# Optimization experiments

Hardware: AMD Instinct MI355X
Metric: run time of the kernel (lower is better)

The kernel has to match this reference:

```python
import jax, jax.numpy as jnp
import numpy as np

B, S, D = 2, 2048, 2048
NH, NG = 16, 4          # q heads, groups
KVH = NH // NG          # kv heads = 4
HD = D // NH            # head dim = 128
ROPE_THETA = 10000.0


def _rope(t, cos, sin):
    """Rotate pairs along last dim. t: [B,S,D]; cos/sin: [S, D//2]."""
    tr = t.reshape(t.shape[:-1] + (-1, 2))  # [B,S,D/2,2] complex pairs (llama layout)
    xr, xi = tr[..., 0], tr[..., 1]
    c = cos[None, :, :]
    s = sin[None, :, :]
    yr = xr * c - xi * s
    yi = xr * s + xi * c
    return jnp.stack([yr, yi], axis=-1).reshape(t.shape)


def setup_inputs() -> dict:
    key = jax.random.key(0)
    k0, k1, k2, k3, k4 = jax.random.split(key, 5)
    scale = 1.0 / np.sqrt(D)
    x = jax.random.normal(k0, (B, S, D), jnp.float32)
    Wq = jax.random.normal(k1, (D, D), jnp.float32) * scale          # torch Linear: (out,in)
    Wk = jax.random.normal(k2, (D // NG, D), jnp.float32) * scale
    Wv = jax.random.normal(k3, (D // NG, D), jnp.float32) * scale
    Wo = jax.random.normal(k4, (D, D), jnp.float32) * scale
    mask = jnp.triu(jnp.ones((S, S), bool), k=1)[None, None]          # causal: True = masked
    return {"x": x, "Wq": Wq, "Wk": Wk, "Wv": Wv, "Wo": Wo, "mask": mask}


def reference(x, Wq, Wk, Wv, Wo, mask):
    b, s, d = x.shape
    q = x @ Wq.T                                  # [B,S,D]
    k = x @ Wk.T                                  # [B,S,D/NG]
    v = x @ Wv.T
    # repeat_kv: [B,S,KVH,HD] -> repeat each kv head NG times -> [B,S,NH,HD]
    k = jnp.repeat(k.reshape(b, s, KVH, HD), NG, axis=2).reshape(b, s, d)
    v = jnp.repeat(v.reshape(b, s, KVH, HD), NG, axis=2).reshape(b, s, d)
    # RoPE with freqs precomputed over the FULL hidden dim (as in source)
    freqs = 1.0 / (ROPE_THETA ** (jnp.arange(0, d, 2, dtype=jnp.float32) / d))  # [D/2]
    ang = jnp.arange(s, dtype=jnp.float32)[:, None] * freqs[None, :]            # [S,D/2]
    cos, sin = jnp.cos(ang), jnp.sin(ang)
    q = _rope(q, cos, sin)
    k = _rope(k, cos, sin)
    # split heads: [B,NH,S,HD]
    qh = q.reshape(b, s, NH, HD).transpose(0, 2, 1, 3)
    kh = k.reshape(b, s, NH, HD).transpose(0, 2, 1, 3)
    vh = v.reshape(b, s, NH, HD).transpose(0, 2, 1, 3)
    # NOTE: source scales by sqrt(hidden_dim), not sqrt(head_dim)
    scores = jnp.einsum('bhqd,bhkd->bhqk', qh, kh) / jnp.sqrt(jnp.float32(d))
    scores = jnp.where(mask, -jnp.inf, scores)
    probs = jax.nn.softmax(scores, axis=-1)
    out = jnp.einsum('bhqk,bhkd->bhqd', probs, vh)
    out = out.transpose(0, 2, 1, 3).reshape(b, s, d)
    return out @ Wo.T  # dropout is identity in eval
```

## Files before the change

### kernel.cpp

```cpp
#include <hip/hip_runtime.h>
#include <hip/hip_bf16.h>
#include <stdint.h>

typedef unsigned short u16;
typedef u16 u16x4 __attribute__((ext_vector_type(4)));
typedef unsigned u32x4 __attribute__((ext_vector_type(4)));
typedef __bf16 bf16x8 __attribute__((ext_vector_type(8)));
typedef float f32x4 __attribute__((ext_vector_type(4)));
typedef float f32x16 __attribute__((ext_vector_type(16)));

#define DEVI __device__ __forceinline__

DEVI u16 f2b(float f) {
  __hip_bfloat16 h = __float2bfloat16(f);
  return __builtin_bit_cast(u16, h);
}

DEVI unsigned pk2(float lo, float hi) {
  return (unsigned)f2b(lo) | ((unsigned)f2b(hi) << 16);
}

DEVI f32x4 mfma16(bf16x8 a, bf16x8 b, f32x4 c) {
  return __builtin_amdgcn_mfma_f32_16x16x32_bf16(a, b, c, 0, 0, 0);
}

DEVI f32x16 mfma32(bf16x8 a, bf16x8 b, f32x16 c) {
  return __builtin_amdgcn_mfma_f32_32x32x16_bf16(a, b, c, 0, 0, 0);
}

DEVI void gld_lds16(const u16* g, u16* l) {
  __builtin_amdgcn_global_load_lds(
      (const __attribute__((address_space(1))) unsigned int*)g,
      (__attribute__((address_space(3))) unsigned int*)l, 16, 0, 0);
}

__global__ void cvt_all(const float4* __restrict__ x, const float4* __restrict__ wq,
                        const float4* __restrict__ wk, const float4* __restrict__ wv,
                        const float4* __restrict__ wo,
                        u16x4* __restrict__ xb, u16x4* __restrict__ wqb,
                        u16x4* __restrict__ wkb, u16x4* __restrict__ wvb,
                        u16x4* __restrict__ wob) {
  long i = (long)blockIdx.x * 256 + threadIdx.x;
  const float4* src; u16x4* dst; long o;
  if (i < 2097152)      { src = x;  dst = xb;  o = i; }
  else if (i < 3145728) { src = wq; dst = wqb; o = i - 2097152; }
  else if (i < 3407872) { src = wk; dst = wkb; o = i - 3145728; }
  else if (i < 3670016) { src = wv; dst = wvb; o = i - 3407872; }
  else                  { src = wo; dst = wob; o = i - 3670016; }
  float4 v = src[o];
  u16x4 r = { f2b(v.x), f2b(v.y), f2b(v.z), f2b(v.w) };
  dst[o] = r;
}

__global__ void rope_table(float* __restrict__ cosT, float* __restrict__ sinT) {
  int i = blockIdx.x * 256 + threadIdx.x;
  int s = i >> 10, p = i & 1023;
  float freq = exp2f((float)p * -0.012976281620653759f);
  float ang = (float)s * freq;
  float sv, cv;
  __sincosf(ang, &sv, &cv);
  cosT[i] = cv;
  sinT[i] = sv;
}

__global__ __launch_bounds__(256)
void gemm_qkv(const u16* __restrict__ A, const u16* __restrict__ wq,
              const u16* __restrict__ wk, const u16* __restrict__ wv,
              float* __restrict__ Qtmp, float* __restrict__ Ktmp,
              u16* __restrict__ Vtp) {
  __shared__ __align__(16) u16 lds[2][2][4096];
  const int tid = threadIdx.x;
  const int lane = tid & 63;
  const int w = tid >> 6;
  const int wr = w >> 1, wc = w & 1;
  const int bx = blockIdx.x;
  const int m0 = blockIdx.y << 7, n0 = bx << 7;
  const int K = 2048;

  const u16* Bw;
  int mode;
  if (bx < 16)      { Bw = wq + (size_t)n0 * K;          mode = 0; }
  else if (bx < 20) { Bw = wk + (size_t)(n0 - 2048) * K; mode = 1; }
  else              { Bw = wv + (size_t)(n0 - 2560) * K; mode = 2; }

  const int srow = tid >> 2;
  const int schunk = (tid & 3) << 3;
  const u16* ga0 = A + (size_t)(m0 + srow) * K + schunk;
  const u16* gb0 = Bw + (size_t)srow * K + schunk;
  const size_t rstep = (size_t)64 * K;

  f32x4 acc[4][4] = {};
  const int nk = K >> 5;
  int cur = 0;

  {
    u16* la = &lds[0][0][tid << 3];
    u16* lb = &lds[0][1][tid << 3];
    gld_lds16(ga0, la);
    gld_lds16(ga0 + rstep, la + 2048);
    gld_lds16(gb0, lb);
    gld_lds16(gb0 + rstep, lb + 2048);
  }
  __syncthreads();

  const int l15 = lane & 15;
  const int kcol = (lane >> 4) << 3;
  const int arow = ((wr << 6) + l15) << 5;
  const int brow = ((wc << 6) + l15) << 5;

  for (int kt = 0; kt < nk; ++kt) {
    if (kt + 1 < nk) {
      const u16* ga = ga0 + ((size_t)(kt + 1) << 5);
      const u16* gb = gb0 + ((size_t)(kt + 1) << 5);
      u16* la = &lds[cur ^ 1][0][tid << 3];
      u16* lb = &lds[cur ^ 1][1][tid << 3];
      gld_lds16(ga, la);
      gld_lds16(ga + rstep, la + 2048);
      gld_lds16(gb, lb);
      gld_lds16(gb + rstep, lb + 2048);
    }
    const u16* la = &lds[cur][0][0];
    const u16* lb = &lds[cur][1][0];
    bf16x8 af[4], bfr[4];
#pragma unroll
    for (int mi = 0; mi < 4; ++mi)
      af[mi] = *(const bf16x8*)&la[arow + (mi << 9) + kcol];
#pragma unroll
    for (int ni = 0; ni < 4; ++ni)
      bfr[ni] = *(const bf16x8*)&lb[brow + (ni << 9) + kcol];
#pragma unroll
    for (int mi = 0; mi < 4; ++mi)
#pragma unroll
      for (int ni = 0; ni < 4; ++ni)
        acc[mi][ni] = mfma16(af[mi], bfr[ni], acc[mi][ni]);
    __syncthreads();
    cur ^= 1;
  }

  const int crow = (lane >> 4) << 2;
  const int ccol = lane & 15;
  if (mode == 0) {
#pragma unroll
    for (int mi = 0; mi < 4; ++mi) {
      int row = m0 + (wr << 6) + (mi << 4) + crow;
#pragma unroll
      for (int ni = 0; ni < 4; ++ni) {
        int col = n0 + (wc << 6) + (ni << 4) + ccol;
#pragma unroll
        for (int rr = 0; rr < 4; ++rr)
          Qtmp[(size_t)(row + rr) * 2048 + col] = acc[mi][ni][rr];
      }
    }
  } else if (mode == 1) {
#pragma unroll
    for (int mi = 0; mi < 4; ++mi) {
      int row = m0 + (wr << 6) + (mi << 4) + crow;
#pragma unroll
      for (int ni = 0; ni < 4; ++ni) {
        int col = (n0 - 2048) + (wc << 6) + (ni << 4) + ccol;
#pragma unroll
        for (int rr = 0; rr < 4; ++rr)
          Ktmp[(size_t)(row + rr) * 512 + col] = acc[mi][ni][rr];
      }
    }
  } else {
#pragma unroll
    for (int mi = 0; mi < 4; ++mi) {
      int sg = m0 + (wr << 6) + (mi << 4) + crow;
      int b = sg >> 11, s = sg & 2047;
#pragma unroll
      for (int ni = 0; ni < 4; ++ni) {
        int n = (n0 - 2560) + (wc << 6) + (ni << 4) + ccol;
        u16x4 pk = { f2b(acc[mi][ni][0]), f2b(acc[mi][ni][1]),
                     f2b(acc[mi][ni][2]), f2b(acc[mi][ni][3]) };
        *(u16x4*)&Vtp[((size_t)((b << 2) + (n >> 7)) * 128 + (n & 127)) * 2048 + s] = pk;
      }
    }
  }
}

__global__ __launch_bounds__(256)
void gemm_bt(const u16* __restrict__ A, const u16* __restrict__ Bw,
             float* __restrict__ C, int M, int N, int K) {
  __shared__ __align__(16) u16 lds[2][2][4096];
  const int tid = threadIdx.x;
  const int lane = tid & 63;
  const int w = tid >> 6;
  const int wr = w >> 1, wc = w & 1;
  const int m0 = blockIdx.y << 7, n0 = blockIdx.x << 7;

  const int srow = tid >> 2;
  const int schunk = (tid & 3) << 3;
  const u16* ga0 = A + (size_t)(m0 + srow) * K + schunk;
  const u16* gb0 = Bw + (size_t)(n0 + srow) * K + schunk;
  const size_t rstep = (size_t)64 * K;

  f32x4 acc[4][4] = {};
  const int nk = K >> 5;
  int cur = 0;

  {
    u16* la = &lds[0][0][tid << 3];
    u16* lb = &lds[0][1][tid << 3];
    gld_lds16(ga0, la);
    gld_lds16(ga0 + rstep, la + 2048);
    gld_lds16(gb0, lb);
    gld_lds16(gb0 + rstep, lb + 2048);
  }
  __syncthreads();

  const int l15 = lane & 15;
  const int kcol = (lane >> 4) << 3;
  const int arow = ((wr << 6) + l15) << 5;
  const int brow = ((wc << 6) + l15) << 5;

  for (int kt = 0; kt < nk; ++kt) {
    if (kt + 1 < nk) {
      const u16* ga = ga0 + ((size_t)(kt + 1) << 5);
      const u16* gb = gb0 + ((size_t)(kt + 1) << 5);
      u16* la = &lds[cur ^ 1][0][tid << 3];
      u16* lb = &lds[cur ^ 1][1][tid << 3];
      gld_lds16(ga, la);
      gld_lds16(ga + rstep, la + 2048);
      gld_lds16(gb, lb);
      gld_lds16(gb + rstep, lb + 2048);
    }
    const u16* la = &lds[cur][0][0];
    const u16* lb = &lds[cur][1][0];
    bf16x8 af[4], bfr[4];
#pragma unroll
    for (int mi = 0; mi < 4; ++mi)
      af[mi] = *(const bf16x8*)&la[arow + (mi << 9) + kcol];
#pragma unroll
    for (int ni = 0; ni < 4; ++ni)
      bfr[ni] = *(const bf16x8*)&lb[brow + (ni << 9) + kcol];
#pragma unroll
    for (int mi = 0; mi < 4; ++mi)
#pragma unroll
      for (int ni = 0; ni < 4; ++ni)
        acc[mi][ni] = mfma16(af[mi], bfr[ni], acc[mi][ni]);
    __syncthreads();
    cur ^= 1;
  }

  const int crow = (lane >> 4) << 2;
  const int ccol = lane & 15;
#pragma unroll
  for (int mi = 0; mi < 4; ++mi) {
    int row = m0 + (wr << 6) + (mi << 4) + crow;
#pragma unroll
    for (int ni = 0; ni < 4; ++ni) {
      int col = n0 + (wc << 6) + (ni << 4) + ccol;
#pragma unroll
      for (int rr = 0; rr < 4; ++rr)
        C[(size_t)(row + rr) * N + col] = acc[mi][ni][rr];
    }
  }
}

__global__ void rope_q(const float2* __restrict__ Qtmp, const float* __restrict__ cosT,
                       const float* __restrict__ sinT, u16* __restrict__ Qh) {
  int i = blockIdx.x * 256 + threadIdx.x;
  int pr = i & 1023;
  int row = i >> 10;
  int s = row & 2047, b = row >> 11;
  float2 v = Qtmp[(size_t)row * 1024 + pr];
  float c = cosT[(s << 10) + pr], sn = sinT[(s << 10) + pr];
  const float SC = 0.022097086912079608f * 1.4426950408889634f;
  float yr = (v.x * c - v.y * sn) * SC;
  float yi = (v.x * sn + v.y * c) * SC;
  int h = pr >> 6, hp = pr & 63;
  size_t off = ((size_t)(b * 16 + h) * 2048 + s) * 128 + hp * 2;
  unsigned pk = (unsigned)f2b(yr) | ((unsigned)f2b(yi) << 16);
  *(unsigned*)&Qh[off] = pk;
}

__global__ void rope_k(const float2* __restrict__ Ktmp, const float* __restrict__ cosT,
                       const float* __restrict__ sinT, u16* __restrict__ Kh) {
  int i = blockIdx.x * 256 + threadIdx.x;
  int hp = i & 63;
  int h = (i >> 6) & 15;
  int row = i >> 10;
  int s = row & 2047, b = row >> 11;
  float2 v = Ktmp[(size_t)row * 256 + ((h >> 2) << 6) + hp];
  int p = (h << 6) + hp;
  float c = cosT[(s << 10) + p], sn = sinT[(s << 10) + p];
  float yr = v.x * c - v.y * sn;
  float yi = v.x * sn + v.y * c;
  size_t off = ((size_t)(b * 16 + h) * 2048 + s) * 128 + hp * 2;
  unsigned pk = (unsigned)f2b(yr) | ((unsigned)f2b(yi) << 16);
  *(unsigned*)&Kh[off] = pk;
}

__global__ __launch_bounds__(256, 2)
void attn_kernel(const u16* __restrict__ Qh, const u16* __restrict__ Kh,
                 const u16* __restrict__ Vt, u16* __restrict__ attnO) {
  __shared__ __align__(16) u16 lds[3][8192];
  const int tid = threadIdx.x, lane = tid & 63, w = tid >> 6;
  const int bid = blockIdx.x;
  const int x = bid & 7, j = bid >> 3;
  const int half = j >> 5, jj = j & 31;
  const int bh = (x << 2) + (jj >> 4) + (half << 1);
  const int r = jj & 15;
  const int qt = half ? r : 15 - r;
  const int h = bh & 15, b = bh >> 4;

  const int qi = lane & 31, hi = lane >> 5;
  const int q0 = (qt << 7) + (w << 5);
  const int qabs = q0 + qi;

  const u16* Qp = Qh + (size_t)(b * 16 + h) * 262144;
  const u16* Kp = Kh + (size_t)(b * 16 + h) * 262144;
  const u16* Vp = Vt + (size_t)((b << 2) + (h >> 2)) * 262144;

  bf16x8 qf[8];
#pragma unroll
  for (int kc = 0; kc < 8; ++kc)
    qf[kc] = *(const bf16x8*)&Qp[(size_t)qabs * 128 + kc * 16 + hi * 8];

  const int kRow = tid >> 4;
  const int kCl = ((tid & 15) ^ (kRow & 7)) << 3;
  const int vRow = tid >> 2;
  const int vCl = ((tid & 3) ^ ((tid >> 3) & 3)) << 3;
  const int ldsoff = tid << 3;

  f32x16 ot[4] = {};
  float mrow = -1e30f, lsum = 0.f;
  const int nt = (qt << 2) + 4;
  const int nt_w = (qt << 2) + w + 1;
  const int swq = qi & 7, swv = (qi >> 1) & 3;

#pragma unroll
  for (int pt = 0; pt < 2; ++pt) {
    u16* bb = (u16*)lds[pt];
    gld_lds16(Kp + (size_t)((pt << 5) + kRow) * 128 + kCl, bb + ldsoff);
    gld_lds16(Kp + (size_t)((pt << 5) + kRow + 16) * 128 + kCl, bb + ldsoff + 2048);
    gld_lds16(Vp + (size_t)vRow * 2048 + (pt << 5) + vCl, bb + 4096 + ldsoff);
    gld_lds16(Vp + (size_t)(vRow + 64) * 2048 + (pt << 5) + vCl, bb + 4096 + ldsoff + 2048);
  }

  int bufc = 0;
  for (int t = 0; t < nt; ++t) {
    asm volatile("s_waitcnt vmcnt(4)" ::: "memory");
    __builtin_amdgcn_sched_barrier(0);
    __builtin_amdgcn_s_barrier();
    {
      const int ts = (t + 2 < nt) ? t + 2 : nt - 1;
      const int bufn = bufc ? bufc - 1 : 2;
      u16* bb = (u16*)lds[bufn];
      gld_lds16(Kp + (size_t)((ts << 5) + kRow) * 128 + kCl, bb + ldsoff);
      gld_lds16(Kp + (size_t)((ts << 5) + kRow + 16) * 128 + kCl, bb + ldsoff + 2048);
      gld_lds16(Vp + (size_t)vRow * 2048 + (ts << 5) + vCl, bb + 4096 + ldsoff);
      gld_lds16(Vp + (size_t)(vRow + 64) * 2048 + (ts << 5) + vCl, bb + 4096 + ldsoff + 2048);
    }
    if (t < nt_w) {
      const u16* kb_ = &lds[bufc][0];
      const u16* vb_ = &lds[bufc][4096];
      f32x16 st = {};
      __builtin_amdgcn_s_setprio(1);
#pragma unroll
      for (int kc = 0; kc < 8; ++kc) {
        bf16x8 kf = *(const bf16x8*)&kb_[(qi << 7) + ((((kc << 1) + hi) ^ swq) << 3)];
        st = mfma32(kf, qf[kc], st);
      }
      __builtin_amdgcn_s_setprio(0);

      if (t == nt_w - 1) {
        const int kb0 = t << 5;
#pragma unroll
        for (int reg = 0; reg < 16; ++reg) {
          int kk = kb0 + (reg & 3) + ((reg >> 2) << 3) + (hi << 2);
          if (kk > qabs) st[reg] = -1e30f;
        }
      }

      float tmax = st[0];
#pragma unroll
      for (int reg = 1; reg < 16; ++reg) tmax = fmaxf(tmax, st[reg]);
      tmax = fmaxf(tmax, __shfl_xor(tmax, 32));

      if (__any(tmax - mrow > 11.5f)) {
        float nm = fmaxf(mrow, tmax);
        float al = __builtin_amdgcn_exp2f(mrow - nm);
        mrow = nm;
        lsum *= al;
#pragma unroll
        for (int db = 0; db < 4; ++db)
#pragma unroll
          for (int reg = 0; reg < 16; ++reg) ot[db][reg] *= al;
      }

      float psum = 0.f;
#pragma unroll
      for (int reg = 0; reg < 16; ++reg) {
        st[reg] = __builtin_amdgcn_exp2f(st[reg] - mrow);
        psum += st[reg];
      }
      psum += __shfl_xor(psum, 32);
      lsum += psum;

      bf16x8 pfrag[2];
#pragma unroll
      for (int bbp = 0; bbp < 2; ++bbp) {
        unsigned x0 = pk2(st[8 * bbp + 0], st[8 * bbp + 1]);
        unsigned x1 = pk2(st[8 * bbp + 2], st[8 * bbp + 3]);
        unsigned y0 = pk2(st[8 * bbp + 4], st[8 * bbp + 5]);
        unsigned y1 = pk2(st[8 * bbp + 6], st[8 * bbp + 7]);
        asm("v_permlane32_swap_b32 %0, %1" : "+v"(x0), "+v"(y0));
        asm("v_permlane32_swap_b32 %0, %1" : "+v"(x1), "+v"(y1));
        u32x4 uw = { x0, x1, y0, y1 };
        pfrag[bbp] = __builtin_bit_cast(bf16x8, uw);
      }

      __builtin_amdgcn_s_setprio(1);
#pragma unroll
      for (int db = 0; db < 4; ++db) {
        const u16* vr = &vb_[((db << 5) + qi) << 5];
#pragma unroll
        for (int ks = 0; ks < 2; ++ks) {
          bf16x8 vf = *(const bf16x8*)&vr[((((ks << 1) + hi)) ^ swv) << 3];
          ot[db] = mfma32(vf, pfrag[ks], ot[db]);
        }
      }
      __builtin_amdgcn_s_setprio(0);
    }
    bufc = (bufc == 2) ? 0 : bufc + 1;
  }

  float inv = 1.f / lsum;
  u16* rowp = attnO + (size_t)(b * 2048 + qabs) * 2048 + h * 128 + (hi << 2);
#pragma unroll
  for (int db = 0; db < 4; ++db)
#pragma unroll
    for (int mg = 0; mg < 4; ++mg) {
      u16x4 pkv = { f2b(ot[db][4 * mg + 0] * inv), f2b(ot[db][4 * mg + 1] * inv),
                    f2b(ot[db][4 * mg + 2] * inv), f2b(ot[db][4 * mg + 3] * inv) };
      *(u16x4*)&rowp[(db << 5) + (mg << 3)] = pkv;
    }
}

extern "C" void kernel_launch(void* const* d_in, const int* in_sizes, int n_in,
                              void* d_out, int out_size, void* d_ws, size_t ws_size,
                              hipStream_t stream) {
  const float* x  = (const float*)d_in[0];
  const float* Wq = (const float*)d_in[1];
  const float* Wk = (const float*)d_in[2];
  const float* Wv = (const float*)d_in[3];
  const float* Wo = (const float*)d_in[4];
  float* out = (float*)d_out;
  char* ws = (char*)d_ws;

  u16*   xb   = (u16*)(ws + 0);
  u16*   wqb  = (u16*)(ws + 16777216);
  u16*   wkb  = (u16*)(ws + 25165824);
  u16*   wvb  = (u16*)(ws + 27262976);
  u16*   wob  = (u16*)(ws + 29360128);
  float* cosT = (float*)(ws + 37748736);
  float* sinT = (float*)(ws + 46137344);
  float* Qtmp = (float*)(ws + 54525952);
  u16*   attnb= (u16*)(ws + 54525952);
  float* Ktmp = (float*)(ws + 88080384);
  u16*   Qhp  = (u16*)(ws + 96468992);
  u16*   Khp  = (u16*)(ws + 113246208);
  u16*   Vtp  = (u16*)(ws + 130023424);

  cvt_all<<<18432, 256, 0, stream>>>((const float4*)x, (const float4*)Wq,
                                     (const float4*)Wk, (const float4*)Wv,
                                     (const float4*)Wo, (u16x4*)xb, (u16x4*)wqb,
                                     (u16x4*)wkb, (u16x4*)wvb, (u16x4*)wob);
  rope_table<<<8192, 256, 0, stream>>>(cosT, sinT);
  gemm_qkv<<<dim3(24, 32), 256, 0, stream>>>(xb, wqb, wkb, wvb, Qtmp, Ktmp, Vtp);
  rope_q<<<16384, 256, 0, stream>>>((const float2*)Qtmp, cosT, sinT, Qhp);
  rope_k<<<16384, 256, 0, stream>>>((const float2*)Ktmp, cosT, sinT, Khp);
  attn_kernel<<<512, 256, 0, stream>>>(Qhp, Khp, Vtp, attnb);
  gemm_bt<<<dim3(16, 32), 256, 0, stream>>>(attnb, wob, out, 4096, 2048, 2048);
}
```

Measured before the change: 229.4 us.

## Fuse RoPE into QKV GEMM epilogue, triple-buffer GEMMs, swizzle block order

Applies RoPE, the softmax scale and the head-split layout directly in the QKV GEMM epilogue, using lane shuffles to pair elements. This removes the fp32 Q/K intermediates and the separate rope_q/rope_k kernels, which were memory-bound round trips. Both GEMMs move to a three-stage LDS pipeline with explicit vmcnt waits, a single barrier per step and raised priority around the MFMAs, and use a swizzled 1D block order for better cache locality. The cos/sin table is interleaved into float2. The K epilogue now writes four replicated heads per element with scattered 4-byte stores, and the larger LDS footprint may lower occupancy.

```diff
diff --git a/kernel.cpp b/kernel.cpp
--- a/kernel.cpp
+++ b/kernel.cpp
@@ -52,36 +52,38 @@
   dst[o] = r;
 }
 
-__global__ void rope_table(float* __restrict__ cosT, float* __restrict__ sinT) {
+__global__ void rope_table(float2* __restrict__ csT) {
   int i = blockIdx.x * 256 + threadIdx.x;
   int s = i >> 10, p = i & 1023;
   float freq = exp2f((float)p * -0.012976281620653759f);
   float ang = (float)s * freq;
   float sv, cv;
   __sincosf(ang, &sv, &cv);
-  cosT[i] = cv;
-  sinT[i] = sv;
+  csT[i] = make_float2(cv, sv);
 }
 
 __global__ __launch_bounds__(256)
 void gemm_qkv(const u16* __restrict__ A, const u16* __restrict__ wq,
               const u16* __restrict__ wk, const u16* __restrict__ wv,
-              float* __restrict__ Qtmp, float* __restrict__ Ktmp,
-              u16* __restrict__ Vtp) {
-  __shared__ __align__(16) u16 lds[2][2][4096];
+              const float2* __restrict__ csT, u16* __restrict__ Qh,
+              u16* __restrict__ Kh, u16* __restrict__ Vtp) {
+  __shared__ __align__(16) u16 lds[3][8192];
   const int tid = threadIdx.x;
   const int lane = tid & 63;
   const int w = tid >> 6;
   const int wr = w >> 1, wc = w & 1;
-  const int bx = blockIdx.x;
-  const int m0 = blockIdx.y << 7, n0 = bx << 7;
+
+  const int fb = blockIdx.x;
+  const int swz = (fb & 7) * 96 + (fb >> 3);
+  const int x = swz % 24, y = swz / 24;
+  const int m0 = y << 7, n0 = x << 7;
   const int K = 2048;
 
   const u16* Bw;
   int mode;
-  if (bx < 16)      { Bw = wq + (size_t)n0 * K;          mode = 0; }
-  else if (bx < 20) { Bw = wk + (size_t)(n0 - 2048) * K; mode = 1; }
-  else              { Bw = wv + (size_t)(n0 - 2560) * K; mode = 2; }
+  if (x < 16)      { Bw = wq + (size_t)n0 * K;          mode = 0; }
+  else if (x < 20) { Bw = wk + (size_t)(n0 - 2048) * K; mode = 1; }
+  else             { Bw = wv + (size_t)(n0 - 2560) * K; mode = 2; }
 
   const int srow = tid >> 2;
   const int schunk = (tid & 3) << 3;
@@ -91,36 +93,38 @@
 
   f32x4 acc[4][4] = {};
   const int nk = K >> 5;
-  int cur = 0;
-
-  {
-    u16* la = &lds[0][0][tid << 3];
-    u16* lb = &lds[0][1][tid << 3];
-    gld_lds16(ga0, la);
-    gld_lds16(ga0 + rstep, la + 2048);
-    gld_lds16(gb0, lb);
-    gld_lds16(gb0 + rstep, lb + 2048);
-  }
-  __syncthreads();
+
+#define QKV_STAGE(buf, ks)                                        \
+  {                                                               \
+    u16* la_ = &lds[buf][tid << 3];                               \
+    const u16* ga_ = ga0 + ((size_t)(ks) << 5);                   \
+    const u16* gb_ = gb0 + ((size_t)(ks) << 5);                   \
+    gld_lds16(ga_, la_);                                          \
+    gld_lds16(ga_ + rstep, la_ + 2048);                           \
+    gld_lds16(gb_, la_ + 4096);                                   \
+    gld_lds16(gb_ + rstep, la_ + 6144);                           \
+  }
+
+  QKV_STAGE(0, 0);
+  QKV_STAGE(1, 1);
 
   const int l15 = lane & 15;
   const int kcol = (lane >> 4) << 3;
   const int arow = ((wr << 6) + l15) << 5;
   const int brow = ((wc << 6) + l15) << 5;
 
+  int bufc = 0;
   for (int kt = 0; kt < nk; ++kt) {
-    if (kt + 1 < nk) {
-      const u16* ga = ga0 + ((size_t)(kt + 1) << 5);
-      const u16* gb = gb0 + ((size_t)(kt + 1) << 5);
-      u16* la = &lds[cur ^ 1][0][tid << 3];
-      u16* lb = &lds[cur ^ 1][1][tid << 3];
-      gld_lds16(ga, la);
-      gld_lds16(ga + rstep, la + 2048);
-      gld_lds16(gb, lb);
-      gld_lds16(gb + rstep, lb + 2048);
-    }
-    const u16* la = &lds[cur][0][0];
-    const u16* lb = &lds[cur][1][0];
+    asm volatile("s_waitcnt vmcnt(4)" ::: "memory");
+    __builtin_amdgcn_sched_barrier(0);
+    __builtin_amdgcn_s_barrier();
+    {
+      const int ts = (kt + 2 < nk) ? kt + 2 : nk - 1;
+      const int bufn = bufc ? bufc - 1 : 2;
+      QKV_STAGE(bufn, ts);
+    }
+    const u16* la = &lds[bufc][0];
+    const u16* lb = &lds[bufc][4096];
     bf16x8 af[4], bfr[4];
 #pragma unroll
     for (int mi = 0; mi < 4; ++mi)
@@ -128,41 +132,66 @@
 #pragma unroll
     for (int ni = 0; ni < 4; ++ni)
       bfr[ni] = *(const bf16x8*)&lb[brow + (ni << 9) + kcol];
+    __builtin_amdgcn_s_setprio(1);
 #pragma unroll
     for (int mi = 0; mi < 4; ++mi)
 #pragma unroll
       for (int ni = 0; ni < 4; ++ni)
         acc[mi][ni] = mfma16(af[mi], bfr[ni], acc[mi][ni]);
-    __syncthreads();
-    cur ^= 1;
-  }
+    __builtin_amdgcn_s_setprio(0);
+    bufc = (bufc == 2) ? 0 : bufc + 1;
+  }
+  asm volatile("s_waitcnt vmcnt(0)" ::: "memory");
 
   const int crow = (lane >> 4) << 2;
   const int ccol = lane & 15;
   if (mode == 0) {
-#pragma unroll
-    for (int mi = 0; mi < 4; ++mi) {
-      int row = m0 + (wr << 6) + (mi << 4) + crow;
-#pragma unroll
-      for (int ni = 0; ni < 4; ++ni) {
-        int col = n0 + (wc << 6) + (ni << 4) + ccol;
-#pragma unroll
-        for (int rr = 0; rr < 4; ++rr)
-          Qtmp[(size_t)(row + rr) * 2048 + col] = acc[mi][ni][rr];
-      }
-    }
+    const float SCL = 0.022097086912079608f * 1.4426950408889634f;
+#pragma unroll
+    for (int mi = 0; mi < 4; ++mi)
+#pragma unroll
+      for (int rr = 0; rr < 4; ++rr) {
+        int row = m0 + (wr << 6) + (mi << 4) + crow + rr;
+        int s = row & 2047, b = row >> 11;
+#pragma unroll
+        for (int ni = 0; ni < 4; ++ni) {
+          int col = n0 + (wc << 6) + (ni << 4) + ccol;
+          float v = acc[mi][ni][rr];
+          float o = __shfl_xor(v, 1);
+          float2 cs = csT[(s << 10) + (col >> 1)];
+          float res = (lane & 1) ? (o * cs.y + v * cs.x) : (v * cs.x - o * cs.y);
+          res *= SCL;
+          float other = __shfl_xor(res, 1);
+          if (!(lane & 1)) {
+            int h = col >> 7, hd = col & 127;
+            *(unsigned*)&Qh[((size_t)(b * 16 + h) * 2048 + s) * 128 + hd] = pk2(res, other);
+          }
+        }
+      }
   } else if (mode == 1) {
 #pragma unroll
-    for (int mi = 0; mi < 4; ++mi) {
-      int row = m0 + (wr << 6) + (mi << 4) + crow;
-#pragma unroll
-      for (int ni = 0; ni < 4; ++ni) {
-        int col = (n0 - 2048) + (wc << 6) + (ni << 4) + ccol;
-#pragma unroll
-        for (int rr = 0; rr < 4; ++rr)
-          Ktmp[(size_t)(row + rr) * 512 + col] = acc[mi][ni][rr];
-      }
-    }
+    for (int mi = 0; mi < 4; ++mi)
+#pragma unroll
+      for (int rr = 0; rr < 4; ++rr) {
+        int row = m0 + (wr << 6) + (mi << 4) + crow + rr;
+        int s = row & 2047, b = row >> 11;
+#pragma unroll
+        for (int ni = 0; ni < 4; ++ni) {
+          int col = (n0 - 2048) + (wc << 6) + (ni << 4) + ccol;
+          float v = acc[mi][ni][rr];
+          float o = __shfl_xor(v, 1);
+          int kvh = col >> 7, hd = col & 127;
+#pragma unroll
+          for (int g = 0; g < 4; ++g) {
+            int h = (kvh << 2) + g;
+            float2 cs = csT[(s << 10) + (h << 6) + (hd >> 1)];
+            float res = (lane & 1) ? (o * cs.y + v * cs.x) : (v * cs.x - o * cs.y);
+            float other = __shfl_xor(res, 1);
+            if (!(lane & 1))
+              *(unsigned*)&Kh[((size_t)(b * 16 + h) * 2048 + s) * 128 + hd] = pk2(res, other);
+          }
+        }
+      }
   } else {
 #pragma unroll
     for (int mi = 0; mi < 4; ++mi) {
@@ -177,17 +206,25 @@
       }
     }
   }
+#undef QKV_STAGE
 }
 
 __global__ __launch_bounds__(256)
 void gemm_bt(const u16* __restrict__ A, const u16* __restrict__ Bw,
              float* __restrict__ C, int M, int N, int K) {
-  __shared__ __align__(16) u16 lds[2][2][4096];
+  __shared__ __align__(16) u16 lds[3][8192];
   const int tid = threadIdx.x;
   const int lane = tid & 63;
   const int w = tid >> 6;
   const int wr = w >> 1, wc = w & 1;
-  const int m0 = blockIdx.y << 7, n0 = blockIdx.x << 7;
+
+  const int nbx = N >> 7;
+  const int nwg = (M >> 7) * nbx;
+  const int cpx = nwg >> 3;
+  const int fb = blockIdx.x;
+  const int swz = (fb & 7) * cpx + (fb >> 3);
+  const int x = swz % nbx, y = swz / nbx;
+  const int m0 = y << 7, n0 = x << 7;
 
   const int srow = tid >> 2;
   const int schunk = (tid & 3) << 3;
@@ -197,36 +234,38 @@
 
   f32x4 acc[4][4] = {};
   const int nk = K >> 5;
-  int cur = 0;
-
-  {
-    u16* la = &lds[0][0][tid << 3];
-    u16* lb = &lds[0][1][tid << 3];
-    gld_lds16(ga0, la);
-    gld_lds16(ga0 + rstep, la + 2048);
-    gld_lds16(gb0, lb);
-    gld_lds16(gb0 + rstep, lb + 2048);
-  }
-  __syncthreads();
+
+#define BT_STAGE(buf, ks)                                         \
+  {                                                               \
+    u16* la_ = &lds[buf][tid << 3];                               \
+    const u16* ga_ = ga0 + ((size_t)(ks) << 5);                   \
+    const u16* gb_ = gb0 + ((size_t)(ks) << 5);                   \
+    gld_lds16(ga_, la_);                                          \
+    gld_lds16(ga_ + rstep, la_ + 2048);                           \
+    gld_lds16(gb_, la_ + 4096);                                   \
+    gld_lds16(gb_ + rstep, la_ + 6144);                           \
+  }
+
+  BT_STAGE(0, 0);
+  BT_STAGE(1, 1);
 
   const int l15 = lane & 15;
   const int kcol = (lane >> 4) << 3;
   const int arow = ((wr << 6) + l15) << 5;
   const int brow = ((wc << 6) + l15) << 5;
 
+  int bufc = 0;
   for (int kt = 0; kt < nk; ++kt) {
-    if (kt + 1 < nk) {
-      const u16* ga = ga0 + ((size_t)(kt + 1) << 5);
-      const u16* gb = gb0 + ((size_t)(kt + 1) << 5);
-      u16* la = &lds[cur ^ 1][0][tid << 3];
-      u16* lb = &lds[cur ^ 1][1][tid << 3];
-      gld_lds16(ga, la);
-      gld_lds16(ga + rstep, la + 2048);
-      gld_lds16(gb, lb);
-      gld_lds16(gb + rstep, lb + 2048);
-    }
-    const u16* la = &lds[cur][0][0];
-    const u16* lb = &lds[cur][1][0];
+    asm volatile("s_waitcnt vmcnt(4)" ::: "memory");
+    __builtin_amdgcn_sched_barrier(0);
+    __builtin_amdgcn_s_barrier();
+    {
+      const int ts = (kt + 2 < nk) ? kt + 2 : nk - 1;
+      const int bufn = bufc ? bufc - 1 : 2;
+      BT_STAGE(bufn, ts);
+    }
+    const u16* la = &lds[bufc][0];
+    const u16* lb = &lds[bufc][4096];
     bf16x8 af[4], bfr[4];
 #pragma unroll
     for (int mi = 0; mi < 4; ++mi)
@@ -234,14 +273,16 @@
 #pragma unroll
     for (int ni = 0; ni < 4; ++ni)
       bfr[ni] = *(const bf16x8*)&lb[brow + (ni << 9) + kcol];
+    __builtin_amdgcn_s_setprio(1);
 #pragma unroll
     for (int mi = 0; mi < 4; ++mi)
 #pragma unroll
       for (int ni = 0; ni < 4; ++ni)
         acc[mi][ni] = mfma16(af[mi], bfr[ni], acc[mi][ni]);
-    __syncthreads();
-    cur ^= 1;
-  }
+    __builtin_amdgcn_s_setprio(0);
+    bufc = (bufc == 2) ? 0 : bufc + 1;
+  }
+  asm volatile("s_waitcnt vmcnt(0)" ::: "memory");
 
   const int crow = (lane >> 4) << 2;
   const int ccol = lane & 15;
@@ -256,40 +297,7 @@
         C[(size_t)(row + rr) * N + col] = acc[mi][ni][rr];
     }
   }
-}
-
-__global__ void rope_q(const float2* __restrict__ Qtmp, const float* __restrict__ cosT,
-                       const float* __restrict__ sinT, u16* __restrict__ Qh) {
-  int i = blockIdx.x * 256 + threadIdx.x;
-  int pr = i & 1023;
-  int row = i >> 10;
-  int s = row & 2047, b = row >> 11;
-  float2 v = Qtmp[(size_t)row * 1024 + pr];
-  float c = cosT[(s << 10) + pr], sn = sinT[(s << 10) + pr];
-  const float SC = 0.022097086912079608f * 1.4426950408889634f;
-  float yr = (v.x * c - v.y * sn) * SC;
-  float yi = (v.x * sn + v.y * c) * SC;
-  int h = pr >> 6, hp = pr & 63;
-  size_t off = ((size_t)(b * 16 + h) * 2048 + s) * 128 + hp * 2;
-  unsigned pk = (unsigned)f2b(yr) | ((unsigned)f2b(yi) << 16);
-  *(unsigned*)&Qh[off] = pk;
-}
-
-__global__ void rope_k(const float2* __restrict__ Ktmp, const float* __restrict__ cosT,
-                       const float* __restrict__ sinT, u16* __restrict__ Kh) {
-  int i = blockIdx.x * 256 + threadIdx.x;
-  int hp = i & 63;
-  int h = (i >> 6) & 15;
-  int row = i >> 10;
-  int s = row & 2047, b = row >> 11;
-  float2 v = Ktmp[(size_t)row * 256 + ((h >> 2) << 6) + hp];
-  int p = (h << 6) + hp;
-  float c = cosT[(s << 10) + p], sn = sinT[(s << 10) + p];
-  float yr = v.x * c - v.y * sn;
-  float yi = v.x * sn + v.y * c;
-  size_t off = ((size_t)(b * 16 + h) * 2048 + s) * 128 + hp * 2;
-  unsigned pk = (unsigned)f2b(yr) | ((unsigned)f2b(yi) << 16);
-  *(unsigned*)&Kh[off] = pk;
+#undef BT_STAGE
 }
 
 __global__ __launch_bounds__(256, 2)
@@ -450,28 +458,23 @@
   float* out = (float*)d_out;
   char* ws = (char*)d_ws;
 
-  u16*   xb   = (u16*)(ws + 0);
-  u16*   wqb  = (u16*)(ws + 16777216);
-  u16*   wkb  = (u16*)(ws + 25165824);
-  u16*   wvb  = (u16*)(ws + 27262976);
-  u16*   wob  = (u16*)(ws + 29360128);
-  float* cosT = (float*)(ws + 37748736);
-  float* sinT = (float*)(ws + 46137344);
-  float* Qtmp = (float*)(ws + 54525952);
-  u16*   attnb= (u16*)(ws + 54525952);
-  float* Ktmp = (float*)(ws + 88080384);
-  u16*   Qhp  = (u16*)(ws + 96468992);
-  u16*   Khp  = (u16*)(ws + 113246208);
-  u16*   Vtp  = (u16*)(ws + 130023424);
+  u16*    xb   = (u16*)(ws + 0);
+  u16*    wqb  = (u16*)(ws + 16777216);
+  u16*    wkb  = (u16*)(ws + 25165824);
+  u16*    wvb  = (u16*)(ws + 27262976);
+  u16*    wob  = (u16*)(ws + 29360128);
+  float2* csT  = (float2*)(ws + 37748736);
+  u16*    Qhp  = (u16*)(ws + 54525952);
+  u16*    Khp  = (u16*)(ws + 71303168);
+  u16*    Vtp  = (u16*)(ws + 88080384);
+  u16*    attnb= (u16*)(ws + 92274688);
 
   cvt_all<<<18432, 256, 0, stream>>>((const float4*)x, (const float4*)Wq,
                                      (const float4*)Wk, (const float4*)Wv,
                                      (const float4*)Wo, (u16x4*)xb, (u16x4*)wqb,
                                      (u16x4*)wkb, (u16x4*)wvb, (u16x4*)wob);
-  rope_table<<<8192, 256, 0, stream>>>(cosT, sinT);
-  gemm_qkv<<<dim3(24, 32), 256, 0, stream>>>(xb, wqb, wkb, wvb, Qtmp, Ktmp, Vtp);
-  rope_q<<<16384, 256, 0, stream>>>((const float2*)Qtmp, cosT, sinT, Qhp);
-  rope_k<<<16384, 256, 0, stream>>>((const float2*)Ktmp, cosT, sinT, Khp);
+  rope_table<<<8192, 256, 0, stream>>>(csT);
+  gemm_qkv<<<768, 256, 0, stream>>>(xb, wqb, wkb, wvb, csT, Qhp, Khp, Vtp);
   attn_kernel<<<512, 256, 0, stream>>>(Qhp, Khp, Vtp, attnb);
-  gemm_bt<<<dim3(16, 32), 256, 0, stream>>>(attnb, wob, out, 4096, 2048, 2048);
-}
+  gemm_bt<<<512, 256, 0, stream>>>(attnb, wob, out, 4096, 2048, 2048);
+}
```

After: 266.4 us. 16.2% more time.
